# Performance work log

Measured on AMD Instinct MI355X. Metric: run time of the kernel, lower is better.

## Reference

```python
import jax, jax.numpy as jnp
import numpy as np
from jax import lax

EPS = 1e-5


def _dcn_core(value, offset, mask, offset_scale):
    # value: (B,H,W,G,D); offset: (B,H,W,G,K,2) as (dx,dy); mask: (B,H,W,G,K)
    # DCNv4: no softmax on mask; sampling loc = center + (kernel_grid + offset)*offset_scale
    B, H, W, G, D = value.shape
    K = mask.shape[-1]
    P = H * W
    kr = jnp.arange(3, dtype=value.dtype) - 1.0
    gy, gx = jnp.meshgrid(kr, kr, indexing="ij")  # 3x3 kernel grid
    gx = gx.reshape(1, 1, 1, 1, K)
    gy = gy.reshape(1, 1, 1, 1, K)
    bx = jnp.arange(W, dtype=value.dtype).reshape(1, 1, W, 1, 1)
    by = jnp.arange(H, dtype=value.dtype).reshape(1, H, 1, 1, 1)
    ix = bx + (gx + offset[..., 0]) * offset_scale  # (B,H,W,G,K) pixel-index coords
    iy = by + (gy + offset[..., 1]) * offset_scale

    tog = lambda a: a.transpose(0, 3, 1, 2, 4).reshape(B, G, P, K)
    ix, iy, m = tog(ix), tog(iy), tog(mask)
    vflat = value.transpose(0, 3, 1, 2, 4).reshape(B, G, P, D)

    x0 = jnp.floor(ix)
    y0 = jnp.floor(iy)
    tx = ix - x0
    ty = iy - y0
    out = jnp.zeros((B, G, P, D), value.dtype)
    # bilinear with zero padding (grid_sample padding_mode='zeros', align_corners=False)
    for dy, dx, wgt in ((0, 0, (1 - ty) * (1 - tx)), (0, 1, (1 - ty) * tx),
                        (1, 0, ty * (1 - tx)), (1, 1, ty * tx)):
        xc = x0 + dx
        yc = y0 + dy
        valid = ((xc >= 0) & (xc < W) & (yc >= 0) & (yc < H)).astype(value.dtype)
        lin = (jnp.clip(yc, 0, H - 1) * W + jnp.clip(xc, 0, W - 1)).astype(jnp.int32)
        v = jnp.take_along_axis(vflat, lin.reshape(B, G, P * K, 1), axis=2)
        v = v.reshape(B, G, P, K, D)
        out = out + jnp.einsum("bgpk,bgpkd->bgpd", wgt * m * valid, v)
    return out.transpose(0, 2, 1, 3).reshape(B, P, G * D)


def setup_inputs() -> dict:
    key = jax.random.key(0)
    ks = jax.random.split(key, 6)
    C = 64
    r = lambda k, shp, s: jax.random.normal(k, shp, jnp.float32) * s
    return {
        "x": r(ks[0], (8, C, 128, 128), 1.0),
        "vp_w": r(ks[1], (C, C), C ** -0.5),
        "vp_b": jnp.zeros((C,), jnp.float32),
        "dw_w": r(ks[2], (C, 1, 3, 3), 1.0 / 3.0),
        "dw_b": jnp.zeros((C,), jnp.float32),
        "om_w": r(ks[3], (56, C), 0.01),
        "om_b": jnp.zeros((56,), jnp.float32),
        "op_w": r(ks[4], (C, C), C ** -0.5),
        "op_b": jnp.zeros((C,), jnp.float32),
        "bn_g": jnp.ones((C // 2,), jnp.float32),
        "bn_b": jnp.zeros((C // 2,), jnp.float32),
        "bn_m": jnp.zeros((C // 2,), jnp.float32),
        "bn_v": jnp.ones((C // 2,), jnp.float32),
    }


def reference(x, vp_w, vp_b, dw_w, dw_b, om_w, om_b, op_w, op_b, bn_g, bn_b, bn_m, bn_v):
    B, C, H, W = x.shape
    G, K, OS = 2, 9, 2.0  # group = in_planes//out_planes = 2; 3x3 -> K=9
    seq = x.reshape(B, H * W, C)  # raw reshape exactly as the torch code
    # DCNv4 value_proj
    val = seq @ vp_w.T + vp_b
    value = val.reshape(B, H, W, G, C // G)
    # offset/mask branch: depthwise 3x3 conv on raw input, then linear
    xi = seq.reshape(B, H, W, C).transpose(0, 3, 1, 2)  # (B,C,H,W)
    dw = lax.conv_general_dilated(xi, dw_w, (1, 1), "SAME",
                                  dimension_numbers=("NCHW", "OIHW", "NCHW"),
                                  feature_group_count=C)
    dw = dw + dw_b[None, :, None, None]
    om = dw.transpose(0, 2, 3, 1) @ om_w.T + om_b  # (B,H,W,56)
    om = om[..., : G * K * 3].reshape(B, H, W, G, 3 * K)  # drop pad-to-8 tail
    offset = om[..., : 2 * K].reshape(B, H, W, G, K, 2)
    mask = om[..., 2 * K:]
    core = _dcn_core(value, offset, mask, OS)  # (B, HW, C)
    out = (core @ op_w.T + op_b).reshape(B, C, H, W)  # raw reshape, as in torch code
    z = 0.5 * (out[:, : C // 2] + out[:, C // 2:])  # chunk + average
    z = bn_g[:, None, None] * (z - bn_m[:, None, None]) * lax.rsqrt(bn_v + EPS)[:, None, None] + bn_b[:, None, None]
    return jnp.maximum(z, 0.0)
```

## Files before the change

### kernel.cpp

```cpp
#include <hip/hip_runtime.h>

#define B_ 8
#define H_ 128
#define W_ 128
#define P_ 16384
#define C_ 64
#define NQ (B_*P_)

static __device__ __forceinline__ void fma4s(float4& a, float s, const float4& v) {
  a.x += s * v.x; a.y += s * v.y; a.z += s * v.z; a.w += s * v.w;
}
static __device__ __forceinline__ void fma4e(float4& a, const float4& u, const float4& v) {
  a.x += u.x * v.x; a.y += u.y * v.y; a.z += u.z * v.z; a.w += u.w * v.w;
}

__global__ __launch_bounds__(256) void gemm64_kernel(
    const float* __restrict__ X, const float* __restrict__ W,
    const float* __restrict__ bias, float* __restrict__ Y) {
  __shared__ __align__(16) float Ws[64][68];
  __shared__ __align__(16) float XsT[64][68];
  int tid = threadIdx.x;
  size_t row0 = (size_t)blockIdx.x * 64;
#pragma unroll
  for (int i0 = 0; i0 < 4096; i0 += 1024) {
    int i = i0 + tid * 4;
    int a = i >> 6, k = i & 63;
    float4 wv = *(const float4*)(W + i);
    Ws[k][a] = wv.x; Ws[k + 1][a] = wv.y; Ws[k + 2][a] = wv.z; Ws[k + 3][a] = wv.w;
    float4 xv = *(const float4*)(X + row0 * 64 + i);
    XsT[k][a] = xv.x; XsT[k + 1][a] = xv.y; XsT[k + 2][a] = xv.z; XsT[k + 3][a] = xv.w;
  }
  __syncthreads();
  int ty = tid >> 4, tx = tid & 15;
  int r0 = ty * 4, c0 = tx * 4;
  float4 b4 = *(const float4*)(bias + c0);
  float4 acc0 = b4, acc1 = b4, acc2 = b4, acc3 = b4;
#pragma unroll 8
  for (int k = 0; k < 64; ++k) {
    float4 wv = *(const float4*)&Ws[k][c0];
    float4 xv = *(const float4*)&XsT[k][r0];
    fma4s(acc0, xv.x, wv);
    fma4s(acc1, xv.y, wv);
    fma4s(acc2, xv.z, wv);
    fma4s(acc3, xv.w, wv);
  }
  float* yb = Y + (row0 + r0) * 64 + c0;
  *(float4*)(yb) = acc0;
  *(float4*)(yb + 64) = acc1;
  *(float4*)(yb + 128) = acc2;
  *(float4*)(yb + 192) = acc3;
}

__global__ __launch_bounds__(256) void dwom_kernel(
    const float* __restrict__ X, const float* __restrict__ dw_w,
    const float* __restrict__ dw_b, const float* __restrict__ om_w,
    const float* __restrict__ om_b, float* __restrict__ OM) {
  __shared__ __align__(16) float dwsT[64][68];
  __shared__ __align__(16) float omwT[64][60];
  __shared__ __align__(16) float dwwT[9][68];
  __shared__ __align__(16) float dwbs[64];
  __shared__ __align__(16) float ombs[56];
  int tid = threadIdx.x;
  for (int i = tid; i < 3456; i += 256) omwT[i & 63][i >> 6] = om_w[i];
  for (int i = tid; i < 576; i += 256) dwwT[i % 9][i / 9] = dw_w[i];
  if (tid < 64) dwbs[tid] = dw_b[tid];
  if (tid < 56) ombs[tid] = (tid < 54) ? om_b[tid] : 0.f;
  int q0 = blockIdx.x * 64;
  int b = q0 >> 14;
  int p0 = q0 & 16383;
  int h = p0 >> 7, w0 = p0 & 127;
  __syncthreads();

  {
    int cv = tid & 15;
    int lqq = tid >> 4;
    int c0 = cv * 4;
    const float* xb = X + (size_t)b * 1048576;
    float4 wt[9];
#pragma unroll
    for (int t = 0; t < 9; ++t) wt[t] = *(const float4*)&dwwT[t][c0];
    float4 dwb4 = *(const float4*)&dwbs[c0];
#pragma unroll
    for (int it = 0; it < 4; ++it) {
      int lq = lqq + 16 * it;
      int ww = w0 + lq;
      float4 acc = dwb4;
#pragma unroll
      for (int t = 0; t < 9; ++t) {
        int dy = t / 3 - 1, dx = t % 3 - 1;
        int hh = h + dy, wx = ww + dx;
        if ((unsigned)hh < 128u && (unsigned)wx < 128u) {
          float4 v = *(const float4*)(xb + (((size_t)(hh * 128 + wx)) << 6) + c0);
          fma4e(acc, v, wt[t]);
        }
      }
      dwsT[c0][lq] = acc.x; dwsT[c0 + 1][lq] = acc.y;
      dwsT[c0 + 2][lq] = acc.z; dwsT[c0 + 3][lq] = acc.w;
    }
  }
  __syncthreads();

  int ty = tid >> 4, tx = tid & 15;
  int r0 = ty * 4, o0 = tx * 4;
  if (o0 < 54) {
    float4 b4 = *(const float4*)&ombs[o0];
    float4 acc0 = b4, acc1 = b4, acc2 = b4, acc3 = b4;
#pragma unroll 8
    for (int k = 0; k < 64; ++k) {
      float4 ov = *(const float4*)&omwT[k][o0];
      float4 dv = *(const float4*)&dwsT[k][r0];
      fma4s(acc0, dv.x, ov);
      fma4s(acc1, dv.y, ov);
      fma4s(acc2, dv.z, ov);
      fma4s(acc3, dv.w, ov);
    }
    float accs[4][4] = {{acc0.x, acc0.y, acc0.z, acc0.w},
                        {acc1.x, acc1.y, acc1.z, acc1.w},
                        {acc2.x, acc2.y, acc2.z, acc2.w},
                        {acc3.x, acc3.y, acc3.z, acc3.w}};
#pragma unroll
    for (int i2 = 0; i2 < 4; i2++) {
      size_t base = (size_t)(q0 + r0 + i2) * 54 + o0;
#pragma unroll
      for (int j = 0; j < 4; j++)
        if (o0 + j < 54) OM[base + j] = accs[i2][j];
    }
  }
}

__global__ __launch_bounds__(256) void dcn_fused_kernel(
    const float* __restrict__ val, const float* __restrict__ OM,
    const float* __restrict__ op_w, const float* __restrict__ op_b,
    const float* __restrict__ bn_g, const float* __restrict__ bn_b,
    const float* __restrict__ bn_m, const float* __restrict__ bn_v,
    float* __restrict__ out) {
  __shared__ __align__(16) float oms[32 * 54];
  __shared__ __align__(16) float cs[32][68];
  __shared__ __align__(16) float Ws[64][68];
  int tid = threadIdx.x;
  int bid = blockIdx.x;
  int b = bid >> 9;
  int p0 = (bid & 511) * 16;
  int q0lo = b * 16384 + p0;

#pragma unroll
  for (int i0 = 0; i0 < 4096; i0 += 1024) {
    int i = i0 + tid * 4;
    int c = i >> 6, k = i & 63;
    float4 wv = *(const float4*)(op_w + i);
    Ws[k][c] = wv.x; Ws[k + 1][c] = wv.y; Ws[k + 2][c] = wv.z; Ws[k + 3][c] = wv.w;
  }
  if (tid < 216) {
    ((float4*)oms)[tid] = ((const float4*)(OM + (size_t)q0lo * 54))[tid];
    ((float4*)(oms + 864))[tid] = ((const float4*)(OM + (size_t)(q0lo + 8192) * 54))[tid];
  }
  __syncthreads();

  {
    int lq = tid >> 4;
    int g = (tid >> 3) & 1;
    int dv = tid & 7;
    const float* vbase = val + (size_t)b * 1048576 + g * 32 + dv * 4;
#pragma unroll
    for (int t = 0; t < 2; ++t) {
      int row = t * 16 + lq;
      int p = p0 + t * 8192 + lq;
      int h = p >> 7, w = p & 127;
      const float* og = oms + row * 54 + g * 27;
      float fw = (float)w, fh = (float)h;
      float4 acc = make_float4(0.f, 0.f, 0.f, 0.f);
#pragma unroll
      for (int k = 0; k < 9; ++k) {
        float offx = og[2 * k], offy = og[2 * k + 1], m = og[18 + k];
        float ix = fw + ((float)(k % 3) - 1.0f + offx) * 2.0f;
        float iy = fh + ((float)(k / 3) - 1.0f + offy) * 2.0f;
        float x0f = floorf(ix), y0f = floorf(iy);
        float tx = ix - x0f, ty = iy - y0f;
        int x0 = (int)x0f, y0 = (int)y0f;
        int x1 = x0 + 1, y1 = y0 + 1;
        float vx0 = ((unsigned)x0 < 128u) ? 1.f : 0.f;
        float vx1 = ((unsigned)x1 < 128u) ? 1.f : 0.f;
        float vy0 = ((unsigned)y0 < 128u) ? 1.f : 0.f;
        float vy1 = ((unsigned)y1 < 128u) ? 1.f : 0.f;
        int xc0 = min(max(x0, 0), 127), xc1 = min(max(x1, 0), 127);
        int yc0 = min(max(y0, 0), 127), yc1 = min(max(y1, 0), 127);
        float w00 = (1.f - ty) * (1.f - tx) * m * vy0 * vx0;
        float w01 = (1.f - ty) * tx * m * vy0 * vx1;
        float w10 = ty * (1.f - tx) * m * vy1 * vx0;
        float w11 = ty * tx * m * vy1 * vx1;
        fma4s(acc, w00, *(const float4*)(vbase + (size_t)((yc0 * 128 + xc0) << 6)));
        fma4s(acc, w01, *(const float4*)(vbase + (size_t)((yc0 * 128 + xc1) << 6)));
        fma4s(acc, w10, *(const float4*)(vbase + (size_t)((yc1 * 128 + xc0) << 6)));
        fma4s(acc, w11, *(const float4*)(vbase + (size_t)((yc1 * 128 + xc1) << 6)));
      }
      *(float4*)&cs[row][g * 32 + dv * 4] = acc;
    }
  }
  __syncthreads();

  int ty = tid >> 4, tx = tid & 15;
  int c0 = tx * 4;
  float4 bias4 = *(const float4*)(op_b + c0);
  float4 accA = bias4, accB = bias4;
#pragma unroll 4
  for (int k0 = 0; k0 < 64; k0 += 4) {
    float4 a4 = *(const float4*)&cs[ty][k0];
    float4 b4 = *(const float4*)&cs[ty + 16][k0];
    float4 w0 = *(const float4*)&Ws[k0][c0];
    float4 w1 = *(const float4*)&Ws[k0 + 1][c0];
    float4 w2 = *(const float4*)&Ws[k0 + 2][c0];
    float4 w3 = *(const float4*)&Ws[k0 + 3][c0];
    fma4s(accA, a4.x, w0); fma4s(accA, a4.y, w1);
    fma4s(accA, a4.z, w2); fma4s(accA, a4.w, w3);
    fma4s(accB, b4.x, w0); fma4s(accB, b4.y, w1);
    fma4s(accB, b4.z, w2); fma4s(accB, b4.w, w3);
  }

  int f = (p0 + ty) * 64 + c0;
  int c2 = f >> 14;
  float scale = bn_g[c2] * rsqrtf(bn_v[c2] + 1e-5f);
  float shift = bn_b[c2] - bn_m[c2] * scale;
  float4 z;
  z.x = fmaxf(0.5f * (accA.x + accB.x) * scale + shift, 0.f);
  z.y = fmaxf(0.5f * (accA.y + accB.y) * scale + shift, 0.f);
  z.z = fmaxf(0.5f * (accA.z + accB.z) * scale + shift, 0.f);
  z.w = fmaxf(0.5f * (accA.w + accB.w) * scale + shift, 0.f);
  *(float4*)(out + (size_t)b * 524288 + f) = z;
}

extern "C" void kernel_launch(void* const* d_in, const int* in_sizes, int n_in,
                              void* d_out, int out_size, void* d_ws, size_t ws_size,
                              hipStream_t stream) {
  const float* x    = (const float*)d_in[0];
  const float* vp_w = (const float*)d_in[1];
  const float* vp_b = (const float*)d_in[2];
  const float* dw_w = (const float*)d_in[3];
  const float* dw_b = (const float*)d_in[4];
  const float* om_w = (const float*)d_in[5];
  const float* om_b = (const float*)d_in[6];
  const float* op_w = (const float*)d_in[7];
  const float* op_b = (const float*)d_in[8];
  const float* bn_g = (const float*)d_in[9];
  const float* bn_b = (const float*)d_in[10];
  const float* bn_m = (const float*)d_in[11];
  const float* bn_v = (const float*)d_in[12];

  float* ws   = (float*)d_ws;
  float* val  = ws;
  float* om   = ws + 16777216;

  gemm64_kernel<<<dim3(NQ / 64), dim3(256), 0, stream>>>(x, vp_w, vp_b, val);
  dwom_kernel<<<dim3(NQ / 64), dim3(256), 0, stream>>>(x, dw_w, dw_b, om_w, om_b, om);
  dcn_fused_kernel<<<dim3(4096), dim3(256), 0, stream>>>(
      val, om, op_w, op_b, bn_g, bn_b, bn_m, bn_v, (float*)d_out);
}
```

Baseline: 132.7 us.

## Store value projection in fp16, enlarge tiles, and swizzle block order

The value projection is now written as fp16, which halves the bytes the bilinear gather in the fused DCN kernel must read. All three kernels handle larger tiles (128 rows per block, 512 threads for the fused kernel) with a block-index swizzle spread across batches. The offset/mask output is stored with vector writes, and the offsets are repacked per group in shared memory. Sampling the value tensor in fp16 adds rounding error, and the larger blocks reduce the number of blocks in flight.

```diff
diff --git a/kernel.cpp b/kernel.cpp
--- a/kernel.cpp
+++ b/kernel.cpp
@@ -7,6 +7,9 @@
 #define C_ 64
 #define NQ (B_*P_)
 
+typedef _Float16 fp16;
+typedef _Float16 half4v __attribute__((ext_vector_type(4)));
+
 static __device__ __forceinline__ void fma4s(float4& a, float s, const float4& v) {
   a.x += s * v.x; a.y += s * v.y; a.z += s * v.z; a.w += s * v.w;
 }
@@ -14,61 +17,80 @@
   a.x += u.x * v.x; a.y += u.y * v.y; a.z += u.z * v.z; a.w += u.w * v.w;
 }
 
-__global__ __launch_bounds__(256) void gemm64_kernel(
+__global__ __launch_bounds__(256) void gemm_val_kernel(
     const float* __restrict__ X, const float* __restrict__ W,
-    const float* __restrict__ bias, float* __restrict__ Y) {
+    const float* __restrict__ bias, fp16* __restrict__ val) {
+  __shared__ __align__(16) float Xs[128][68];
   __shared__ __align__(16) float Ws[64][68];
-  __shared__ __align__(16) float XsT[64][68];
   int tid = threadIdx.x;
-  size_t row0 = (size_t)blockIdx.x * 64;
+  int bid = blockIdx.x;
+  int logical = (bid & 7) * 128 + (bid >> 3);
+  size_t row0 = (size_t)logical * 128;
+
+#pragma unroll
+  for (int i0 = 0; i0 < 8192; i0 += 1024) {
+    int i = i0 + tid * 4;
+    int r = i >> 6, k = i & 63;
+    *(float4*)&Xs[r][k] = *(const float4*)(X + row0 * 64 + i);
+  }
 #pragma unroll
   for (int i0 = 0; i0 < 4096; i0 += 1024) {
     int i = i0 + tid * 4;
-    int a = i >> 6, k = i & 63;
+    int c = i >> 6, k = i & 63;
     float4 wv = *(const float4*)(W + i);
-    Ws[k][a] = wv.x; Ws[k + 1][a] = wv.y; Ws[k + 2][a] = wv.z; Ws[k + 3][a] = wv.w;
-    float4 xv = *(const float4*)(X + row0 * 64 + i);
-    XsT[k][a] = xv.x; XsT[k + 1][a] = xv.y; XsT[k + 2][a] = xv.z; XsT[k + 3][a] = xv.w;
-  }
-  __syncthreads();
+    Ws[k][c] = wv.x; Ws[k + 1][c] = wv.y; Ws[k + 2][c] = wv.z; Ws[k + 3][c] = wv.w;
+  }
+  __syncthreads();
+
   int ty = tid >> 4, tx = tid & 15;
-  int r0 = ty * 4, c0 = tx * 4;
+  int c0 = tx * 4;
   float4 b4 = *(const float4*)(bias + c0);
-  float4 acc0 = b4, acc1 = b4, acc2 = b4, acc3 = b4;
-#pragma unroll 8
-  for (int k = 0; k < 64; ++k) {
-    float4 wv = *(const float4*)&Ws[k][c0];
-    float4 xv = *(const float4*)&XsT[k][r0];
-    fma4s(acc0, xv.x, wv);
-    fma4s(acc1, xv.y, wv);
-    fma4s(acc2, xv.z, wv);
-    fma4s(acc3, xv.w, wv);
-  }
-  float* yb = Y + (row0 + r0) * 64 + c0;
-  *(float4*)(yb) = acc0;
-  *(float4*)(yb + 64) = acc1;
-  *(float4*)(yb + 128) = acc2;
-  *(float4*)(yb + 192) = acc3;
+  float4 acc[8];
+#pragma unroll
+  for (int rr = 0; rr < 8; ++rr) acc[rr] = b4;
+#pragma unroll 4
+  for (int k0 = 0; k0 < 64; k0 += 4) {
+    float4 w0 = *(const float4*)&Ws[k0][c0];
+    float4 w1 = *(const float4*)&Ws[k0 + 1][c0];
+    float4 w2 = *(const float4*)&Ws[k0 + 2][c0];
+    float4 w3 = *(const float4*)&Ws[k0 + 3][c0];
+#pragma unroll
+    for (int rr = 0; rr < 8; ++rr) {
+      float4 xv = *(const float4*)&Xs[ty + rr * 16][k0];
+      fma4s(acc[rr], xv.x, w0); fma4s(acc[rr], xv.y, w1);
+      fma4s(acc[rr], xv.z, w2); fma4s(acc[rr], xv.w, w3);
+    }
+  }
+#pragma unroll
+  for (int rr = 0; rr < 8; ++rr) {
+    int r = ty + rr * 16;
+    half4v hv;
+    hv.x = (fp16)acc[rr].x; hv.y = (fp16)acc[rr].y;
+    hv.z = (fp16)acc[rr].z; hv.w = (fp16)acc[rr].w;
+    *(half4v*)(val + (row0 + r) * 64 + c0) = hv;
+  }
 }
 
 __global__ __launch_bounds__(256) void dwom_kernel(
     const float* __restrict__ X, const float* __restrict__ dw_w,
     const float* __restrict__ dw_b, const float* __restrict__ om_w,
     const float* __restrict__ om_b, float* __restrict__ OM) {
-  __shared__ __align__(16) float dwsT[64][68];
+  __shared__ __align__(16) float dws[128][68];
   __shared__ __align__(16) float omwT[64][60];
   __shared__ __align__(16) float dwwT[9][68];
   __shared__ __align__(16) float dwbs[64];
   __shared__ __align__(16) float ombs[56];
   int tid = threadIdx.x;
+  int bid = blockIdx.x;
+  int logical = (bid & 7) * 128 + (bid >> 3);
+  int q0 = logical * 128;
+  int b = q0 >> 14;
+  int h = logical & 127;
+
   for (int i = tid; i < 3456; i += 256) omwT[i & 63][i >> 6] = om_w[i];
   for (int i = tid; i < 576; i += 256) dwwT[i % 9][i / 9] = dw_w[i];
   if (tid < 64) dwbs[tid] = dw_b[tid];
   if (tid < 56) ombs[tid] = (tid < 54) ? om_b[tid] : 0.f;
-  int q0 = blockIdx.x * 64;
-  int b = q0 >> 14;
-  int p0 = q0 & 16383;
-  int h = p0 >> 7, w0 = p0 & 127;
   __syncthreads();
 
   {
@@ -81,78 +103,90 @@
     for (int t = 0; t < 9; ++t) wt[t] = *(const float4*)&dwwT[t][c0];
     float4 dwb4 = *(const float4*)&dwbs[c0];
 #pragma unroll
-    for (int it = 0; it < 4; ++it) {
+    for (int it = 0; it < 8; ++it) {
       int lq = lqq + 16 * it;
-      int ww = w0 + lq;
       float4 acc = dwb4;
 #pragma unroll
       for (int t = 0; t < 9; ++t) {
         int dy = t / 3 - 1, dx = t % 3 - 1;
-        int hh = h + dy, wx = ww + dx;
+        int hh = h + dy, wx = lq + dx;
         if ((unsigned)hh < 128u && (unsigned)wx < 128u) {
           float4 v = *(const float4*)(xb + (((size_t)(hh * 128 + wx)) << 6) + c0);
           fma4e(acc, v, wt[t]);
         }
       }
-      dwsT[c0][lq] = acc.x; dwsT[c0 + 1][lq] = acc.y;
-      dwsT[c0 + 2][lq] = acc.z; dwsT[c0 + 3][lq] = acc.w;
+      *(float4*)&dws[lq][c0] = acc;
     }
   }
   __syncthreads();
 
   int ty = tid >> 4, tx = tid & 15;
-  int r0 = ty * 4, o0 = tx * 4;
+  int o0 = tx * 4;
   if (o0 < 54) {
     float4 b4 = *(const float4*)&ombs[o0];
-    float4 acc0 = b4, acc1 = b4, acc2 = b4, acc3 = b4;
-#pragma unroll 8
-    for (int k = 0; k < 64; ++k) {
-      float4 ov = *(const float4*)&omwT[k][o0];
-      float4 dv = *(const float4*)&dwsT[k][r0];
-      fma4s(acc0, dv.x, ov);
-      fma4s(acc1, dv.y, ov);
-      fma4s(acc2, dv.z, ov);
-      fma4s(acc3, dv.w, ov);
-    }
-    float accs[4][4] = {{acc0.x, acc0.y, acc0.z, acc0.w},
-                        {acc1.x, acc1.y, acc1.z, acc1.w},
-                        {acc2.x, acc2.y, acc2.z, acc2.w},
-                        {acc3.x, acc3.y, acc3.z, acc3.w}};
-#pragma unroll
-    for (int i2 = 0; i2 < 4; i2++) {
-      size_t base = (size_t)(q0 + r0 + i2) * 54 + o0;
-#pragma unroll
-      for (int j = 0; j < 4; j++)
-        if (o0 + j < 54) OM[base + j] = accs[i2][j];
-    }
-  }
-}
-
-__global__ __launch_bounds__(256) void dcn_fused_kernel(
-    const float* __restrict__ val, const float* __restrict__ OM,
+    float4 acc[8];
+#pragma unroll
+    for (int rr = 0; rr < 8; ++rr) acc[rr] = b4;
+#pragma unroll 4
+    for (int k0 = 0; k0 < 64; k0 += 4) {
+      float4 w0 = *(const float4*)&omwT[k0][o0];
+      float4 w1 = *(const float4*)&omwT[k0 + 1][o0];
+      float4 w2 = *(const float4*)&omwT[k0 + 2][o0];
+      float4 w3 = *(const float4*)&omwT[k0 + 3][o0];
+#pragma unroll
+      for (int rr = 0; rr < 8; ++rr) {
+        float4 dv = *(const float4*)&dws[ty + rr * 16][k0];
+        fma4s(acc[rr], dv.x, w0); fma4s(acc[rr], dv.y, w1);
+        fma4s(acc[rr], dv.z, w2); fma4s(acc[rr], dv.w, w3);
+      }
+    }
+#pragma unroll
+    for (int rr = 0; rr < 8; ++rr) {
+      int r = ty + rr * 16;
+      size_t base = (size_t)(q0 + r) * 54 + o0;
+      if (o0 <= 48) {
+        *(float4*)(OM + base) = acc[rr];
+      } else {
+        *(float2*)(OM + base) = make_float2(acc[rr].x, acc[rr].y);
+      }
+    }
+  }
+}
+
+__global__ __launch_bounds__(512, 4) void dcn_fused_kernel(
+    const fp16* __restrict__ val, const float* __restrict__ OM,
     const float* __restrict__ op_w, const float* __restrict__ op_b,
     const float* __restrict__ bn_g, const float* __restrict__ bn_b,
     const float* __restrict__ bn_m, const float* __restrict__ bn_v,
     float* __restrict__ out) {
-  __shared__ __align__(16) float oms[32 * 54];
-  __shared__ __align__(16) float cs[32][68];
+  __shared__ __align__(16) float oms2[128 * 2 * 28];
+  __shared__ __align__(16) float cs[128][68];
   __shared__ __align__(16) float Ws[64][68];
   int tid = threadIdx.x;
   int bid = blockIdx.x;
-  int b = bid >> 9;
-  int p0 = (bid & 511) * 16;
+  int logical = (bid & 7) * 128 + (bid >> 3);
+  int b = logical >> 7;
+  int p0 = (logical & 127) << 6;
   int q0lo = b * 16384 + p0;
 
 #pragma unroll
-  for (int i0 = 0; i0 < 4096; i0 += 1024) {
+  for (int i0 = 0; i0 < 4096; i0 += 2048) {
     int i = i0 + tid * 4;
     int c = i >> 6, k = i & 63;
     float4 wv = *(const float4*)(op_w + i);
     Ws[k][c] = wv.x; Ws[k + 1][c] = wv.y; Ws[k + 2][c] = wv.z; Ws[k + 3][c] = wv.w;
   }
-  if (tid < 216) {
-    ((float4*)oms)[tid] = ((const float4*)(OM + (size_t)q0lo * 54))[tid];
-    ((float4*)(oms + 864))[tid] = ((const float4*)(OM + (size_t)(q0lo + 8192) * 54))[tid];
+  {
+    const float* srcLo = OM + (size_t)q0lo * 54;
+    const float* srcHi = OM + (size_t)(q0lo + 8192) * 54;
+    for (int j = tid; j < 6912; j += 512) {
+      float v = (j < 3456) ? srcLo[j] : srcHi[j - 3456];
+      int row = j / 54;
+      int o = j - row * 54;
+      int g = o >= 27;
+      int oo = o - 27 * g;
+      oms2[(row * 2 + g) * 28 + oo] = v;
+    }
   }
   __syncthreads();
 
@@ -160,20 +194,22 @@
     int lq = tid >> 4;
     int g = (tid >> 3) & 1;
     int dv = tid & 7;
-    const float* vbase = val + (size_t)b * 1048576 + g * 32 + dv * 4;
-#pragma unroll
-    for (int t = 0; t < 2; ++t) {
-      int row = t * 16 + lq;
-      int p = p0 + t * 8192 + lq;
-      int h = p >> 7, w = p & 127;
-      const float* og = oms + row * 54 + g * 27;
+    const fp16* vbase = val + ((size_t)b << 20) + g * 32 + dv * 4;
+#pragma unroll
+    for (int t = 0; t < 4; ++t) {
+      int row = lq + 32 * t;
+      int hi = row >> 6;
+      int w = (p0 & 127) + (row & 63);
+      int h = (p0 >> 7) + (hi << 6);
+      const float* og = oms2 + (row * 2 + g) * 28;
       float fw = (float)w, fh = (float)h;
       float4 acc = make_float4(0.f, 0.f, 0.f, 0.f);
 #pragma unroll
       for (int k = 0; k < 9; ++k) {
-        float offx = og[2 * k], offy = og[2 * k + 1], m = og[18 + k];
-        float ix = fw + ((float)(k % 3) - 1.0f + offx) * 2.0f;
-        float iy = fh + ((float)(k / 3) - 1.0f + offy) * 2.0f;
+        float2 oxy = *(const float2*)(og + 2 * k);
+        float m = og[18 + k];
+        float ix = fw + ((float)(k % 3) - 1.0f + oxy.x) * 2.0f;
+        float iy = fh + ((float)(k / 3) - 1.0f + oxy.y) * 2.0f;
         float x0f = floorf(ix), y0f = floorf(iy);
         float tx = ix - x0f, ty = iy - y0f;
         int x0 = (int)x0f, y0 = (int)y0f;
@@ -188,44 +224,65 @@
         float w01 = (1.f - ty) * tx * m * vy0 * vx1;
         float w10 = ty * (1.f - tx) * m * vy1 * vx0;
         float w11 = ty * tx * m * vy1 * vx1;
-        fma4s(acc, w00, *(const float4*)(vbase + (size_t)((yc0 * 128 + xc0) << 6)));
-        fma4s(acc, w01, *(const float4*)(vbase + (size_t)((yc0 * 128 + xc1) << 6)));
-        fma4s(acc, w10, *(const float4*)(vbase + (size_t)((yc1 * 128 + xc0) << 6)));
-        fma4s(acc, w11, *(const float4*)(vbase + (size_t)((yc1 * 128 + xc1) << 6)));
+        half4v v00 = *(const half4v*)(vbase + ((size_t)((yc0 * 128 + xc0)) << 6));
+        half4v v01 = *(const half4v*)(vbase + ((size_t)((yc0 * 128 + xc1)) << 6));
+        half4v v10 = *(const half4v*)(vbase + ((size_t)((yc1 * 128 + xc0)) << 6));
+        half4v v11 = *(const half4v*)(vbase + ((size_t)((yc1 * 128 + xc1)) << 6));
+        float4 f00 = {(float)v00.x, (float)v00.y, (float)v00.z, (float)v00.w};
+        float4 f01 = {(float)v01.x, (float)v01.y, (float)v01.z, (float)v01.w};
+        float4 f10 = {(float)v10.x, (float)v10.y, (float)v10.z, (float)v10.w};
+        float4 f11 = {(float)v11.x, (float)v11.y, (float)v11.z, (float)v11.w};
+        fma4s(acc, w00, f00); fma4s(acc, w01, f01);
+        fma4s(acc, w10, f10); fma4s(acc, w11, f11);
       }
       *(float4*)&cs[row][g * 32 + dv * 4] = acc;
     }
   }
   __syncthreads();
 
-  int ty = tid >> 4, tx = tid & 15;
-  int c0 = tx * 4;
-  float4 bias4 = *(const float4*)(op_b + c0);
-  float4 accA = bias4, accB = bias4;
-#pragma unroll 4
-  for (int k0 = 0; k0 < 64; k0 += 4) {
-    float4 a4 = *(const float4*)&cs[ty][k0];
-    float4 b4 = *(const float4*)&cs[ty + 16][k0];
-    float4 w0 = *(const float4*)&Ws[k0][c0];
-    float4 w1 = *(const float4*)&Ws[k0 + 1][c0];
-    float4 w2 = *(const float4*)&Ws[k0 + 2][c0];
-    float4 w3 = *(const float4*)&Ws[k0 + 3][c0];
-    fma4s(accA, a4.x, w0); fma4s(accA, a4.y, w1);
-    fma4s(accA, a4.z, w2); fma4s(accA, a4.w, w3);
-    fma4s(accB, b4.x, w0); fma4s(accB, b4.y, w1);
-    fma4s(accB, b4.z, w2); fma4s(accB, b4.w, w3);
-  }
-
-  int f = (p0 + ty) * 64 + c0;
-  int c2 = f >> 14;
-  float scale = bn_g[c2] * rsqrtf(bn_v[c2] + 1e-5f);
-  float shift = bn_b[c2] - bn_m[c2] * scale;
-  float4 z;
-  z.x = fmaxf(0.5f * (accA.x + accB.x) * scale + shift, 0.f);
-  z.y = fmaxf(0.5f * (accA.y + accB.y) * scale + shift, 0.f);
-  z.z = fmaxf(0.5f * (accA.z + accB.z) * scale + shift, 0.f);
-  z.w = fmaxf(0.5f * (accA.w + accB.w) * scale + shift, 0.f);
-  *(float4*)(out + (size_t)b * 524288 + f) = z;
+  int tyg = tid >> 4;
+  int txg = tid & 15;
+  if (tyg < 16) {
+    int c0 = txg * 4;
+    float4 accL[4], accH[4];
+#pragma unroll
+    for (int m = 0; m < 4; ++m) {
+      accL[m] = make_float4(0.f, 0.f, 0.f, 0.f);
+      accH[m] = make_float4(0.f, 0.f, 0.f, 0.f);
+    }
+#pragma unroll 2
+    for (int k0 = 0; k0 < 64; k0 += 4) {
+      float4 w0 = *(const float4*)&Ws[k0][c0];
+      float4 w1 = *(const float4*)&Ws[k0 + 1][c0];
+      float4 w2 = *(const float4*)&Ws[k0 + 2][c0];
+      float4 w3 = *(const float4*)&Ws[k0 + 3][c0];
+#pragma unroll
+      for (int m = 0; m < 4; ++m) {
+        int r = tyg + 16 * m;
+        float4 aL = *(const float4*)&cs[r][k0];
+        float4 aH = *(const float4*)&cs[r + 64][k0];
+        fma4s(accL[m], aL.x, w0); fma4s(accL[m], aL.y, w1);
+        fma4s(accL[m], aL.z, w2); fma4s(accL[m], aL.w, w3);
+        fma4s(accH[m], aH.x, w0); fma4s(accH[m], aH.y, w1);
+        fma4s(accH[m], aH.z, w2); fma4s(accH[m], aH.w, w3);
+      }
+    }
+    float4 bias4 = *(const float4*)(op_b + c0);
+#pragma unroll
+    for (int m = 0; m < 4; ++m) {
+      int r = tyg + 16 * m;
+      int f = (p0 + r) * 64 + c0;
+      int c2 = f >> 14;
+      float scale = bn_g[c2] * rsqrtf(bn_v[c2] + 1e-5f);
+      float shift = bn_b[c2] - bn_m[c2] * scale;
+      float4 z;
+      z.x = fmaxf((0.5f * (accL[m].x + accH[m].x) + bias4.x) * scale + shift, 0.f);
+      z.y = fmaxf((0.5f * (accL[m].y + accH[m].y) + bias4.y) * scale + shift, 0.f);
+      z.z = fmaxf((0.5f * (accL[m].z + accH[m].z) + bias4.z) * scale + shift, 0.f);
+      z.w = fmaxf((0.5f * (accL[m].w + accH[m].w) + bias4.w) * scale + shift, 0.f);
+      *(float4*)(out + (size_t)b * 524288 + f) = z;
+    }
+  }
 }
 
 extern "C" void kernel_launch(void* const* d_in, const int* in_sizes, int n_in,
@@ -246,11 +303,11 @@
   const float* bn_v = (const float*)d_in[12];
 
   float* ws   = (float*)d_ws;
-  float* val  = ws;
+  fp16* val_h = (fp16*)d_ws;
   float* om   = ws + 16777216;
 
-  gemm64_kernel<<<dim3(NQ / 64), dim3(256), 0, stream>>>(x, vp_w, vp_b, val);
-  dwom_kernel<<<dim3(NQ / 64), dim3(256), 0, stream>>>(x, dw_w, dw_b, om_w, om_b, om);
-  dcn_fused_kernel<<<dim3(4096), dim3(256), 0, stream>>>(
-      val, om, op_w, op_b, bn_g, bn_b, bn_m, bn_v, (float*)d_out);
-}
+  gemm_val_kernel<<<dim3(1024), dim3(256), 0, stream>>>(x, vp_w, vp_b, val_h);
+  dwom_kernel<<<dim3(1024), dim3(256), 0, stream>>>(x, dw_w, dw_b, om_w, om_b, om);
+  dcn_fused_kernel<<<dim3(1024), dim3(512), 0, stream>>>(
+      val_h, om, op_w, op_b, bn_g, bn_b, bn_m, bn_v, (float*)d_out);
+}
```

Result: slower. 136.0 us (+2.5%).
